# Performance work log

Measured on AMD Instinct MI355X. Metric: run time of the kernel, lower is better.

Reference implementation:

```python
import jax, jax.numpy as jnp
import numpy as np

N_NODES = 20000
N_EDGES = 320000
HEADS = 16
NEG_SLOPE = 0.2


def _gat_conv(x, src, dst, W, a_src, a_dst, b, heads, out_ch):
    # x: [N, F_in]; src/dst: [E'] (self-loops already appended)
    N = x.shape[0]
    h = (x @ W).reshape(N, heads, out_ch)                  # [N, H, C]
    alpha_s = jnp.sum(h * a_src, axis=-1)                  # [N, H]
    alpha_d = jnp.sum(h * a_dst, axis=-1)                  # [N, H]
    e = jax.nn.leaky_relu(alpha_s[src] + alpha_d[dst], NEG_SLOPE)  # [E', H]
    # segment softmax over edges grouped by destination node
    m = jax.ops.segment_max(e, dst, num_segments=N)        # [N, H]
    ex = jnp.exp(e - m[dst])
    denom = jax.ops.segment_sum(ex, dst, num_segments=N)
    alpha = ex / (denom[dst] + 1e-16)                      # [E', H]
    msg = h[src] * alpha[:, :, None]                       # [E', H, C]
    out = jax.ops.segment_sum(msg, dst, num_segments=N)    # [N, H, C]
    return out.reshape(N, heads * out_ch) + b


def _forward(x, edge_index, params):
    N = x.shape[0]
    loops = jnp.arange(N, dtype=edge_index.dtype)
    src = jnp.concatenate([edge_index[0], loops])
    dst = jnp.concatenate([edge_index[1], loops])
    for i, (W, a_s, a_d, b, out_ch) in enumerate(params):
        x = _gat_conv(x, src, dst, W, a_s, a_d, b, HEADS, out_ch)
        if i < len(params) - 1:
            x = jax.nn.relu(x)
    return jnp.sum(x, axis=0, keepdims=True)               # [1, 768]


def setup_inputs() -> dict:
    key = jax.random.key(0)
    ks = jax.random.split(key, 32)
    hid, heads, out_c = 64, HEADS, 3
    dims = [(3, hid), (hid * heads, hid), (hid * heads, hid), (hid * heads, hid), (hid * heads, hid), (hid * heads, out_c * heads)]
    inp = {}
    inp["x"] = jax.random.normal(ks[0], (N_NODES, 3), dtype=jnp.float32)
    inp["edge_index"] = jax.random.randint(ks[1], (2, N_EDGES), 0, N_NODES, dtype=jnp.int64)
    k = 2
    for li, (fin, c) in enumerate(dims, start=1):
        inp[f"W{li}"] = jax.random.normal(ks[k], (fin, heads * c), dtype=jnp.float32) * 0.1; k += 1
        inp[f"a{li}s"] = jax.random.normal(ks[k], (heads, c), dtype=jnp.float32) * 0.1; k += 1
        inp[f"a{li}d"] = jax.random.normal(ks[k], (heads, c), dtype=jnp.float32) * 0.1; k += 1
        inp[f"b{li}"] = jnp.zeros((heads * c,), dtype=jnp.float32)
    return inp


def reference(x, edge_index, W1, a1s, a1d, b1, W2, a2s, a2d, b2, W3, a3s, a3d, b3, W4, a4s, a4d, b4, W5, a5s, a5d, b5, W6, a6s, a6d, b6):
    params = [
        (W1, a1s, a1d, b1, 64), (W2, a2s, a2d, b2, 64), (W3, a3s, a3d, b3, 64),
        (W4, a4s, a4d, b4, 64), (W5, a5s, a5d, b5, 64), (W6, a6s, a6d, b6, 48),
    ]
    return _forward(x, edge_index, params)
```

## Files before the change

### kernel.cpp

```cpp
#include <hip/hip_runtime.h>
#include <cstddef>
#include <cstdint>

#define N_NODES 20000
#define N_EDGES 320000
#define E_TOT   (N_EDGES + N_NODES)
#define HEADS   16

typedef __bf16 bf16;
typedef __attribute__((ext_vector_type(8))) __bf16 bf16x8;
typedef __attribute__((ext_vector_type(4))) __bf16 bf16x4;
typedef __attribute__((ext_vector_type(4))) float  f32x4;

__device__ __forceinline__ void gll16(const void* g, void* l) {
    __builtin_amdgcn_global_load_lds(
        (const __attribute__((address_space(1))) unsigned int*)g,
        (__attribute__((address_space(3))) unsigned int*)l, 16, 0, 0);
}

__global__ __launch_bounds__(256)
void k_lin1(const float* __restrict__ x, const float* __restrict__ W,
            const float* __restrict__ aS, const float* __restrict__ aD,
            bf16* __restrict__ hg, float* __restrict__ as_,
            float* __restrict__ ad_) {
    int n = blockIdx.x;
    int t = threadIdx.x;
    int f0 = t * 4, hd = t >> 4;
    float x0 = x[n*3+0], x1 = x[n*3+1], x2 = x[n*3+2];
    float v[4];
    bf16x4 hv;
#pragma unroll
    for (int c = 0; c < 4; ++c) {
        int f = f0 + c;
        v[c] = x0*W[f] + x1*W[1024+f] + x2*W[2048+f];
        hv[c] = (bf16)v[c];
    }
    *reinterpret_cast<bf16x4*>(&hg[(size_t)n * 1024 + f0]) = hv;
    float ps = 0.f, pd = 0.f;
    int cb = (t & 15) * 4;
#pragma unroll
    for (int c = 0; c < 4; ++c) {
        ps = fmaf(v[c], aS[hd*64 + cb + c], ps);
        pd = fmaf(v[c], aD[hd*64 + cb + c], pd);
    }
#pragma unroll
    for (int off = 1; off < 16; off <<= 1) {
        ps += __shfl_xor(ps, off);
        pd += __shfl_xor(pd, off);
    }
    if ((t & 15) == 0) {
        as_[n*16 + hd] = ps;
        ad_[n*16 + hd] = pd;
    }
}

__global__ __launch_bounds__(256)
void k_convW(const float* __restrict__ W, bf16* __restrict__ Th,
             bf16* __restrict__ Tl, int M) {
    __shared__ float t[32][33];
    int m0 = blockIdx.x * 32, k0 = blockIdx.y * 32;
    int j = threadIdx.x & 31, i0 = threadIdx.x >> 5;
#pragma unroll
    for (int s = 0; s < 4; ++s) {
        int i = i0 + s * 8;
        t[i][j] = W[(size_t)(k0 + i) * M + m0 + j];
    }
    __syncthreads();
#pragma unroll
    for (int s = 0; s < 4; ++s) {
        int i = i0 + s * 8;
        float v = t[j][i];
        bf16 hi = (bf16)v;
        Th[(size_t)(m0 + i) * 1024 + k0 + j] = hi;
        if (Tl) Tl[(size_t)(m0 + i) * 1024 + k0 + j] = (bf16)(v - (float)hi);
    }
}

template<bool FUSE, bool TWOB>
__global__ __launch_bounds__(256, 2)
void k_gemm3(const bf16* __restrict__ Ah,
             const bf16* __restrict__ Bh, const bf16* __restrict__ Bl,
             float* __restrict__ Cf, bf16* __restrict__ Ch,
             const float* __restrict__ aS, const float* __restrict__ aD,
             float* __restrict__ as_, float* __restrict__ ad_,
             int N, int M) {
    __shared__ __align__(16) bf16 sAh[128 * 32];
    __shared__ __align__(16) bf16 sBh[128 * 32];
    __shared__ __align__(16) bf16 sBl[TWOB ? 128 * 32 : 8];

    const int tid  = threadIdx.x;
    const int wid  = tid >> 6, lane = tid & 63;
    const int wr   = wid >> 1, wc = wid & 1;
    const int col0 = blockIdx.x * 128, row0 = blockIdx.y * 128;

    f32x4 acc[4][4] = {};

    const int rl = lane >> 2;
    const int gg = lane & 3;
    const int rb0 = wid * 32;
    const int lrow = lane & 15, g4 = lane >> 4;

    for (int k0 = 0; k0 < 1024; k0 += 32) {
#pragma unroll
        for (int half = 0; half < 2; ++half) {
            int rt = rb0 + half * 16 + rl;
            int kc = (gg ^ ((rt >> 1) & 3)) * 8;
            size_t lbase = (size_t)(rb0 + half * 16) * 32;
            int ar = row0 + rt; if (ar >= N) ar = N - 1;
            gll16(Ah + (size_t)ar * 1024 + k0 + kc, sAh + lbase);
            int br = col0 + rt;
            gll16(Bh + (size_t)br * 1024 + k0 + kc, sBh + lbase);
            if (TWOB) gll16(Bl + (size_t)br * 1024 + k0 + kc, sBl + lbase);
        }
        __syncthreads();

        bf16x8 ah[4], bh[4], bl[4];
#pragma unroll
        for (int m = 0; m < 4; ++m) {
            int r = wr * 64 + m * 16 + lrow;
            int off = r * 32 + ((g4 ^ ((r >> 1) & 3)) * 8);
            ah[m] = *(const bf16x8*)&sAh[off];
        }
#pragma unroll
        for (int n = 0; n < 4; ++n) {
            int r = wc * 64 + n * 16 + lrow;
            int off = r * 32 + ((g4 ^ ((r >> 1) & 3)) * 8);
            bh[n] = *(const bf16x8*)&sBh[off];
            if (TWOB) bl[n] = *(const bf16x8*)&sBl[off];
        }
#pragma unroll
        for (int m = 0; m < 4; ++m)
#pragma unroll
            for (int n = 0; n < 4; ++n) {
                acc[m][n] = __builtin_amdgcn_mfma_f32_16x16x32_bf16(ah[m], bh[n], acc[m][n], 0, 0, 0);
                if (TWOB)
                    acc[m][n] = __builtin_amdgcn_mfma_f32_16x16x32_bf16(ah[m], bl[n], acc[m][n], 0, 0, 0);
            }
        __syncthreads();
    }

#pragma unroll
    for (int m = 0; m < 4; ++m) {
#pragma unroll
        for (int n = 0; n < 4; ++n) {
            int col = col0 + wc * 64 + n * 16 + lrow;
#pragma unroll
            for (int q = 0; q < 4; ++q) {
                int row = row0 + wr * 64 + m * 16 + g4 * 4 + q;
                if (row < N) {
                    float v = acc[m][n][q];
                    if (!FUSE) Cf[(size_t)row * M + col] = v;
                    Ch[(size_t)row * M + col] = (bf16)v;
                }
            }
        }
    }

    if (FUSE) {
        const int hd = blockIdx.x * 2 + wc;
        float asv[4], adv[4];
#pragma unroll
        for (int n = 0; n < 4; ++n) {
            asv[n] = aS[hd * 64 + n * 16 + lrow];
            adv[n] = aD[hd * 64 + n * 16 + lrow];
        }
        float ps[4][4], pd[4][4];
#pragma unroll
        for (int m = 0; m < 4; ++m)
#pragma unroll
            for (int q = 0; q < 4; ++q) {
                float s = 0.f, d = 0.f;
#pragma unroll
                for (int n = 0; n < 4; ++n) {
                    s = fmaf(acc[m][n][q], asv[n], s);
                    d = fmaf(acc[m][n][q], adv[n], d);
                }
                ps[m][q] = s; pd[m][q] = d;
            }
#pragma unroll
        for (int off = 1; off < 16; off <<= 1) {
#pragma unroll
            for (int m = 0; m < 4; ++m)
#pragma unroll
                for (int q = 0; q < 4; ++q) {
                    ps[m][q] += __shfl_xor(ps[m][q], off);
                    pd[m][q] += __shfl_xor(pd[m][q], off);
                }
        }
        if (lrow == 0) {
#pragma unroll
            for (int m = 0; m < 4; ++m)
#pragma unroll
                for (int q = 0; q < 4; ++q) {
                    int row = row0 + wr * 64 + m * 16 + g4 * 4 + q;
                    if (row < N) {
                        as_[row * 16 + hd] = ps[m][q];
                        ad_[row * 16 + hd] = pd[m][q];
                    }
                }
        }
    }
}

__global__ __launch_bounds__(256)
void k_alpha(const float* __restrict__ h, const float* __restrict__ a_s,
             const float* __restrict__ a_d, float* __restrict__ as_out,
             float* __restrict__ ad_out, int C, int M) {
    int pair = blockIdx.x * 4 + (threadIdx.x >> 6);
    int lane = threadIdx.x & 63;
    if (pair >= N_NODES * HEADS) return;
    int n = pair >> 4, hd = pair & 15;
    float vs = 0.f, vd = 0.f;
    if (lane < C) {
        float hv = h[(size_t)n * M + hd * C + lane];
        vs = hv * a_s[hd * C + lane];
        vd = hv * a_d[hd * C + lane];
    }
#pragma unroll
    for (int off = 32; off > 0; off >>= 1) {
        vs += __shfl_down(vs, off);
        vd += __shfl_down(vd, off);
    }
    if (lane == 0) { as_out[pair] = vs; ad_out[pair] = vd; }
}

__global__ void k_zero_i(int* __restrict__ p, int n) {
    int t = blockIdx.x * 256 + threadIdx.x;
    if (t < n) p[t] = 0;
}
__global__ void k_hist(const int* __restrict__ ei, int* __restrict__ deg) {
    int e = blockIdx.x * 256 + threadIdx.x;
    if (e >= E_TOT) return;
    int d = (e < N_EDGES) ? ei[N_EDGES + e] : e - N_EDGES;
    atomicAdd(&deg[d], 1);
}
__global__ __launch_bounds__(256)
void k_scan(const int* __restrict__ deg, int* __restrict__ rowstart,
            int* __restrict__ cursor) {
    __shared__ int sh[256];
    int carry = 0;
    for (int base = 0; base < N_NODES; base += 256) {
        int i = base + threadIdx.x;
        int v = (i < N_NODES) ? deg[i] : 0;
        sh[threadIdx.x] = v;
        __syncthreads();
        for (int off = 1; off < 256; off <<= 1) {
            int t = (threadIdx.x >= off) ? sh[threadIdx.x - off] : 0;
            __syncthreads();
            sh[threadIdx.x] += t;
            __syncthreads();
        }
        if (i < N_NODES) {
            int excl = carry + sh[threadIdx.x] - v;
            rowstart[i] = excl;
            cursor[i] = excl;
        }
        carry += sh[255];
        __syncthreads();
    }
    if (threadIdx.x == 0) rowstart[N_NODES] = carry;
}
__global__ void k_scatter(const int* __restrict__ ei, int* __restrict__ cursor,
                          int* __restrict__ csr_src) {
    int e = blockIdx.x * 256 + threadIdx.x;
    if (e >= E_TOT) return;
    int s, d;
    if (e < N_EDGES) { s = ei[e]; d = ei[N_EDGES + e]; }
    else             { s = d = e - N_EDGES; }
    int slot = atomicAdd(&cursor[d], 1);
    csr_src[slot] = s;
}

__global__ __launch_bounds__(256)
void k_agg1024(const bf16* __restrict__ hg, const int* __restrict__ rowstart,
               const int* __restrict__ csr_src, const float* __restrict__ as_,
               const float* __restrict__ ad_, const float* __restrict__ bias,
               bf16* __restrict__ oh) {
    int slice = blockIdx.x;
    int n = blockIdx.y * 16 + (threadIdx.x >> 4);
    int sub = threadIdx.x & 15;
    int f0 = slice * 128 + sub * 8;
    int hd = f0 >> 6;
    int s0 = rowstart[n], s1 = rowstart[n + 1];
    float adv = ad_[n * 16 + hd];
    float m = -1e30f, den = 0.f;
    float acc[8] = {};
    for (int j = s0; j < s1; ++j) {
        int s = csr_src[j];
        float v = as_[s * 16 + hd] + adv;
        v = v > 0.f ? v : 0.2f * v;
        bf16x8 hv = *reinterpret_cast<const bf16x8*>(&hg[(size_t)s * 1024 + f0]);
        float nm = fmaxf(m, v);
        float rm = __expf(m - nm);
        float re = __expf(v - nm);
        den = den * rm + re;
#pragma unroll
        for (int c = 0; c < 8; ++c)
            acc[c] = fmaf(acc[c], rm, re * (float)hv[c]);
        m = nm;
    }
    float inv = 1.f / (den + 1e-16f);
    bf16x8 vh;
#pragma unroll
    for (int c = 0; c < 8; ++c) {
        float r = fmaxf(fmaf(acc[c], inv, bias[f0 + c]), 0.f);
        vh[c] = (bf16)r;
    }
    *reinterpret_cast<bf16x8*>(&oh[(size_t)n * 1024 + f0]) = vh;
}

__global__ __launch_bounds__(256)
void k_agg768(const bf16* __restrict__ hg, const int* __restrict__ rowstart,
              const int* __restrict__ csr_src, const float* __restrict__ as_,
              const float* __restrict__ ad_, const float* __restrict__ bias,
              float* __restrict__ out) {
    int n = blockIdx.x * 2 + (threadIdx.x >> 7);
    int tloc = threadIdx.x & 127;
    if (tloc >= 96) return;
    int f0 = tloc * 8;
    int hd = f0 / 48;
    int s0 = rowstart[n], s1 = rowstart[n + 1];
    float adv = ad_[n * 16 + hd];
    float m = -1e30f, den = 0.f;
    float acc[8] = {};
    for (int j = s0; j < s1; ++j) {
        int s = csr_src[j];
        float v = as_[s * 16 + hd] + adv;
        v = v > 0.f ? v : 0.2f * v;
        bf16x8 hv = *reinterpret_cast<const bf16x8*>(&hg[(size_t)s * 768 + f0]);
        float nm = fmaxf(m, v);
        float rm = __expf(m - nm);
        float re = __expf(v - nm);
        den = den * rm + re;
#pragma unroll
        for (int c = 0; c < 8; ++c)
            acc[c] = fmaf(acc[c], rm, re * (float)hv[c]);
        m = nm;
    }
    float inv = 1.f / (den + 1e-16f);
#pragma unroll
    for (int c = 0; c < 8; ++c)
        out[(size_t)n * 768 + f0 + c] = fmaf(acc[c], inv, bias[f0 + c]);
}

__global__ __launch_bounds__(256)
void k_colsum(const float* __restrict__ x, float* __restrict__ out) {
    int f = blockIdx.x * 256 + threadIdx.x;
    int chunk = blockIdx.y;
    int n0 = chunk * 625, n1 = n0 + 625;
    float s = 0.f;
    for (int n = n0; n < n1; ++n) s += x[(size_t)n * 768 + f];
    atomicAdd(&out[f], s);
}

extern "C" void kernel_launch(void* const* d_in, const int* in_sizes, int n_in,
                              void* d_out, int out_size, void* d_ws, size_t ws_size,
                              hipStream_t stream) {
    const float* x0 = (const float*)d_in[0];
    const int*   ei = (const int*)d_in[1];

    char* w = (char*)d_ws;
    float* xB  = (float*)w;
    float* xOut = (float*)w;
    w += (size_t)N_NODES * 1024 * sizeof(float);
    bf16*  hgat = (bf16*)w; w += (size_t)N_NODES * 1024 * sizeof(bf16);
    bf16*  x_hi = (bf16*)w; w += (size_t)N_NODES * 1024 * sizeof(bf16);
    float* as_  = (float*)w; w += (size_t)N_NODES * HEADS * sizeof(float);
    float* ad_  = (float*)w; w += (size_t)N_NODES * HEADS * sizeof(float);
    bf16* Wt_hi = (bf16*)w; w += (size_t)1024 * 1024 * sizeof(bf16);
    bf16* Wt_lo = (bf16*)w; w += (size_t)1024 * 1024 * sizeof(bf16);
    int* deg      = (int*)w; w += N_NODES * sizeof(int);
    int* rowstart = (int*)w; w += (N_NODES + 1) * sizeof(int);
    int* cursor   = (int*)w; w += N_NODES * sizeof(int);
    int* csr_src  = (int*)w; w += E_TOT * sizeof(int);

    k_zero_i<<<(N_NODES + 255) / 256, 256, 0, stream>>>(deg, N_NODES);
    k_hist<<<(E_TOT + 255) / 256, 256, 0, stream>>>(ei, deg);
    k_scan<<<1, 256, 0, stream>>>(deg, rowstart, cursor);
    k_scatter<<<(E_TOT + 255) / 256, 256, 0, stream>>>(ei, cursor, csr_src);

    for (int l = 0; l < 6; ++l) {
        const float* W  = (const float*)d_in[2 + 4 * l + 0];
        const float* aS = (const float*)d_in[2 + 4 * l + 1];
        const float* aD = (const float*)d_in[2 + 4 * l + 2];
        const float* bv = (const float*)d_in[2 + 4 * l + 3];
        int M = (l == 5) ? 768 : 1024;

        if (l == 0) {
            k_lin1<<<N_NODES, 256, 0, stream>>>(x0, W, aS, aD, hgat, as_, ad_);
        } else {
            dim3 tg(M / 32, 32);
            dim3 grid(M / 128, (N_NODES + 127) / 128);
            if (l < 5) {
                k_convW<<<tg, 256, 0, stream>>>(W, Wt_hi, nullptr, M);
                k_gemm3<true, false><<<grid, 256, 0, stream>>>(
                    x_hi, Wt_hi, nullptr, nullptr, hgat, aS, aD, as_, ad_,
                    N_NODES, M);
            } else {
                k_convW<<<tg, 256, 0, stream>>>(W, Wt_hi, Wt_lo, M);
                k_gemm3<false, true><<<grid, 256, 0, stream>>>(
                    x_hi, Wt_hi, Wt_lo, xB, hgat, nullptr, nullptr,
                    nullptr, nullptr, N_NODES, M);
                k_alpha<<<(N_NODES * HEADS + 3) / 4, 256, 0, stream>>>(
                    xB, aS, aD, as_, ad_, 48, 768);
            }
        }
        if (l < 5) {
            dim3 agrid(8, N_NODES / 16);
            k_agg1024<<<agrid, 256, 0, stream>>>(
                hgat, rowstart, csr_src, as_, ad_, bv, x_hi);
        } else {
            k_agg768<<<N_NODES / 2, 256, 0, stream>>>(
                hgat, rowstart, csr_src, as_, ad_, bv, xOut);
        }
    }

    hipMemsetAsync(d_out, 0, (size_t)out_size * sizeof(float), stream);
    dim3 cgrid(3, 32);
    k_colsum<<<cgrid, 256, 0, stream>>>(xOut, (float*)d_out);
}
```

Measured before the change: 1.218 ms.

## Sort nodes by degree for aggregation and software-pipeline neighbor loads

```diff
diff --git a/kernel.cpp b/kernel.cpp
--- a/kernel.cpp
+++ b/kernel.cpp
@@ -271,33 +271,78 @@
     csr_src[slot] = s;
 }
 
+__global__ void k_dhist(const int* __restrict__ deg, int* __restrict__ bins) {
+    int n = blockIdx.x * 256 + threadIdx.x;
+    if (n >= N_NODES) return;
+    int d = deg[n]; if (d > 255) d = 255;
+    atomicAdd(&bins[d], 1);
+}
+__global__ __launch_bounds__(256)
+void k_dscan(const int* __restrict__ bins, int* __restrict__ cur) {
+    __shared__ int sh[256];
+    int v = bins[threadIdx.x];
+    sh[threadIdx.x] = v;
+    __syncthreads();
+    for (int off = 1; off < 256; off <<= 1) {
+        int t = (threadIdx.x >= off) ? sh[threadIdx.x - off] : 0;
+        __syncthreads();
+        sh[threadIdx.x] += t;
+        __syncthreads();
+    }
+    cur[threadIdx.x] = sh[threadIdx.x] - v;
+}
+__global__ void k_dscatter(const int* __restrict__ deg, int* __restrict__ cur,
+                           int* __restrict__ perm) {
+    int n = blockIdx.x * 256 + threadIdx.x;
+    if (n >= N_NODES) return;
+    int d = deg[n]; if (d > 255) d = 255;
+    int slot = atomicAdd(&cur[d], 1);
+    perm[slot] = n;
+}
+
 __global__ __launch_bounds__(256)
 void k_agg1024(const bf16* __restrict__ hg, const int* __restrict__ rowstart,
-               const int* __restrict__ csr_src, const float* __restrict__ as_,
-               const float* __restrict__ ad_, const float* __restrict__ bias,
-               bf16* __restrict__ oh) {
-    int slice = blockIdx.x;
-    int n = blockIdx.y * 16 + (threadIdx.x >> 4);
+               const int* __restrict__ csr_src, const int* __restrict__ perm,
+               const float* __restrict__ as_, const float* __restrict__ ad_,
+               const float* __restrict__ bias, bf16* __restrict__ oh) {
+    int n = perm[blockIdx.y * 16 + (threadIdx.x >> 4)];
     int sub = threadIdx.x & 15;
-    int f0 = slice * 128 + sub * 8;
+    int f0 = blockIdx.x * 128 + sub * 8;
     int hd = f0 >> 6;
     int s0 = rowstart[n], s1 = rowstart[n + 1];
     float adv = ad_[n * 16 + hd];
+
+    int s_cur = csr_src[s0];
+    float as_cur = as_[s_cur * 16 + hd];
+    bf16x8 hv_cur = *reinterpret_cast<const bf16x8*>(&hg[(size_t)s_cur * 1024 + f0]);
+    int jn = (s0 + 1 < s1) ? s0 + 1 : s1 - 1;
+    int s_nxt = csr_src[jn];
+
     float m = -1e30f, den = 0.f;
     float acc[8] = {};
     for (int j = s0; j < s1; ++j) {
-        int s = csr_src[j];
-        float v = as_[s * 16 + hd] + adv;
+        int j2 = (j + 2 < s1) ? j + 2 : s1 - 1;
+        int s_n2 = csr_src[j2];
+        float as_nxt = as_[s_nxt * 16 + hd];
+        bf16x8 hv_nxt = *reinterpret_cast<const bf16x8*>(&hg[(size_t)s_nxt * 1024 + f0]);
+
+        float v = as_cur + adv;
         v = v > 0.f ? v : 0.2f * v;
-        bf16x8 hv = *reinterpret_cast<const bf16x8*>(&hg[(size_t)s * 1024 + f0]);
-        float nm = fmaxf(m, v);
-        float rm = __expf(m - nm);
-        float re = __expf(v - nm);
-        den = den * rm + re;
-#pragma unroll
-        for (int c = 0; c < 8; ++c)
-            acc[c] = fmaf(acc[c], rm, re * (float)hv[c]);
-        m = nm;
+        if (v <= m) {
+            float re = __expf(v - m);
+            den += re;
+#pragma unroll
+            for (int c = 0; c < 8; ++c)
+                acc[c] = fmaf(re, (float)hv_cur[c], acc[c]);
+        } else {
+            float rm = __expf(m - v);
+            den = fmaf(den, rm, 1.f);
+#pragma unroll
+            for (int c = 0; c < 8; ++c)
+                acc[c] = fmaf(acc[c], rm, (float)hv_cur[c]);
+            m = v;
+        }
+        s_cur = s_nxt; as_cur = as_nxt; hv_cur = hv_nxt; s_nxt = s_n2;
     }
     float inv = 1.f / (den + 1e-16f);
     bf16x8 vh;
@@ -311,31 +356,48 @@
 
 __global__ __launch_bounds__(256)
 void k_agg768(const bf16* __restrict__ hg, const int* __restrict__ rowstart,
-              const int* __restrict__ csr_src, const float* __restrict__ as_,
-              const float* __restrict__ ad_, const float* __restrict__ bias,
-              float* __restrict__ out) {
-    int n = blockIdx.x * 2 + (threadIdx.x >> 7);
+              const int* __restrict__ csr_src, const int* __restrict__ perm,
+              const float* __restrict__ as_, const float* __restrict__ ad_,
+              const float* __restrict__ bias, float* __restrict__ out) {
+    int n = perm[blockIdx.x * 2 + (threadIdx.x >> 7)];
     int tloc = threadIdx.x & 127;
     if (tloc >= 96) return;
     int f0 = tloc * 8;
     int hd = f0 / 48;
     int s0 = rowstart[n], s1 = rowstart[n + 1];
     float adv = ad_[n * 16 + hd];
+
+    int s_cur = csr_src[s0];
+    float as_cur = as_[s_cur * 16 + hd];
+    bf16x8 hv_cur = *reinterpret_cast<const bf16x8*>(&hg[(size_t)s_cur * 768 + f0]);
+    int jn = (s0 + 1 < s1) ? s0 + 1 : s1 - 1;
+    int s_nxt = csr_src[jn];
+
     float m = -1e30f, den = 0.f;
     float acc[8] = {};
     for (int j = s0; j < s1; ++j) {
-        int s = csr_src[j];
-        float v = as_[s * 16 + hd] + adv;
+        int j2 = (j + 2 < s1) ? j + 2 : s1 - 1;
+        int s_n2 = csr_src[j2];
+        float as_nxt = as_[s_nxt * 16 + hd];
+        bf16x8 hv_nxt = *reinterpret_cast<const bf16x8*>(&hg[(size_t)s_nxt * 768 + f0]);
+
+        float v = as_cur + adv;
         v = v > 0.f ? v : 0.2f * v;
-        bf16x8 hv = *reinterpret_cast<const bf16x8*>(&hg[(size_t)s * 768 + f0]);
-        float nm = fmaxf(m, v);
-        float rm = __expf(m - nm);
-        float re = __expf(v - nm);
-        den = den * rm + re;
-#pragma unroll
-        for (int c = 0; c < 8; ++c)
-            acc[c] = fmaf(acc[c], rm, re * (float)hv[c]);
-        m = nm;
+        if (v <= m) {
+            float re = __expf(v - m);
+            den += re;
+#pragma unroll
+            for (int c = 0; c < 8; ++c)
+                acc[c] = fmaf(re, (float)hv_cur[c], acc[c]);
+        } else {
+            float rm = __expf(m - v);
+            den = fmaf(den, rm, 1.f);
+#pragma unroll
+            for (int c = 0; c < 8; ++c)
+                acc[c] = fmaf(acc[c], rm, (float)hv_cur[c]);
+            m = v;
+        }
+        s_cur = s_nxt; as_cur = as_nxt; hv_cur = hv_nxt; s_nxt = s_n2;
     }
     float inv = 1.f / (den + 1e-16f);
 #pragma unroll
@@ -373,11 +435,18 @@
     int* rowstart = (int*)w; w += (N_NODES + 1) * sizeof(int);
     int* cursor   = (int*)w; w += N_NODES * sizeof(int);
     int* csr_src  = (int*)w; w += E_TOT * sizeof(int);
+    int* dbins    = (int*)w; w += 256 * sizeof(int);
+    int* dcur     = (int*)w; w += 256 * sizeof(int);
+    int* perm     = (int*)w; w += N_NODES * sizeof(int);
 
     k_zero_i<<<(N_NODES + 255) / 256, 256, 0, stream>>>(deg, N_NODES);
     k_hist<<<(E_TOT + 255) / 256, 256, 0, stream>>>(ei, deg);
     k_scan<<<1, 256, 0, stream>>>(deg, rowstart, cursor);
     k_scatter<<<(E_TOT + 255) / 256, 256, 0, stream>>>(ei, cursor, csr_src);
+    k_zero_i<<<1, 256, 0, stream>>>(dbins, 256);
+    k_dhist<<<(N_NODES + 255) / 256, 256, 0, stream>>>(deg, dbins);
+    k_dscan<<<1, 256, 0, stream>>>(dbins, dcur);
+    k_dscatter<<<(N_NODES + 255) / 256, 256, 0, stream>>>(deg, dcur, perm);
 
     for (int l = 0; l < 6; ++l) {
         const float* W  = (const float*)d_in[2 + 4 * l + 0];
@@ -408,10 +477,10 @@
         if (l < 5) {
             dim3 agrid(8, N_NODES / 16);
             k_agg1024<<<agrid, 256, 0, stream>>>(
-                hgat, rowstart, csr_src, as_, ad_, bv, x_hi);
+                hgat, rowstart, csr_src, perm, as_, ad_, bv, x_hi);
         } else {
             k_agg768<<<N_NODES / 2, 256, 0, stream>>>(
-                hgat, rowstart, csr_src, as_, ad_, bv, xOut);
+                hgat, rowstart, csr_src, perm, as_, ad_, bv, xOut);
         }
     }
 
```

After: 1.247 ms. +2.4%, slower.

## Precompute per-edge softmax attention weights in a separate kernel before aggregation

Applied to the files above, without the earlier changes.

```diff
diff --git a/kernel.cpp b/kernel.cpp
--- a/kernel.cpp
+++ b/kernel.cpp
@@ -272,38 +272,55 @@
 }
 
 __global__ __launch_bounds__(256)
-void k_agg1024(const bf16* __restrict__ hg, const int* __restrict__ rowstart,
-               const int* __restrict__ csr_src, const float* __restrict__ as_,
-               const float* __restrict__ ad_, const float* __restrict__ bias,
-               bf16* __restrict__ oh) {
-    int slice = blockIdx.x;
-    int n = blockIdx.y * 16 + (threadIdx.x >> 4);
-    int sub = threadIdx.x & 15;
-    int f0 = slice * 128 + sub * 8;
-    int hd = f0 >> 6;
+void k_alpha_edge(const int* __restrict__ rowstart, const int* __restrict__ csr_src,
+                  const float* __restrict__ as_, const float* __restrict__ ad_,
+                  float* __restrict__ alpha) {
+    int t = blockIdx.x * 256 + threadIdx.x;
+    if (t >= N_NODES * HEADS) return;
+    int n = t >> 4, hd = t & 15;
     int s0 = rowstart[n], s1 = rowstart[n + 1];
-    float adv = ad_[n * 16 + hd];
+    float adv = ad_[t];
     float m = -1e30f, den = 0.f;
-    float acc[8] = {};
     for (int j = s0; j < s1; ++j) {
-        int s = csr_src[j];
-        float v = as_[s * 16 + hd] + adv;
+        float v = as_[csr_src[j] * 16 + hd] + adv;
         v = v > 0.f ? v : 0.2f * v;
-        bf16x8 hv = *reinterpret_cast<const bf16x8*>(&hg[(size_t)s * 1024 + f0]);
         float nm = fmaxf(m, v);
         float rm = __expf(m - nm);
         float re = __expf(v - nm);
         den = den * rm + re;
+        m = nm;
+    }
+    float inv = 1.f / (den + 1e-16f);
+    for (int j = s0; j < s1; ++j) {
+        float v = as_[csr_src[j] * 16 + hd] + adv;
+        v = v > 0.f ? v : 0.2f * v;
+        alpha[(size_t)j * 16 + hd] = __expf(v - m) * inv;
+    }
+}
+
+__global__ __launch_bounds__(256)
+void k_agg1024(const bf16* __restrict__ hg, const int* __restrict__ rowstart,
+               const int* __restrict__ csr_src, const float* __restrict__ alpha,
+               const float* __restrict__ bias, bf16* __restrict__ oh) {
+    int n = blockIdx.y * 16 + (threadIdx.x >> 4);
+    int sub = threadIdx.x & 15;
+    int f0 = blockIdx.x * 128 + sub * 8;
+    int hd = f0 >> 6;
+    int s0 = rowstart[n], s1 = rowstart[n + 1];
+    float acc[8] = {};
+#pragma unroll 2
+    for (int j = s0; j < s1; ++j) {
+        int s = csr_src[j];
+        float a = alpha[(size_t)j * 16 + hd];
+        bf16x8 hv = *reinterpret_cast<const bf16x8*>(&hg[(size_t)s * 1024 + f0]);
 #pragma unroll
         for (int c = 0; c < 8; ++c)
-            acc[c] = fmaf(acc[c], rm, re * (float)hv[c]);
-        m = nm;
-    }
-    float inv = 1.f / (den + 1e-16f);
+            acc[c] = fmaf(a, (float)hv[c], acc[c]);
+    }
     bf16x8 vh;
 #pragma unroll
     for (int c = 0; c < 8; ++c) {
-        float r = fmaxf(fmaf(acc[c], inv, bias[f0 + c]), 0.f);
+        float r = fmaxf(acc[c] + bias[f0 + c], 0.f);
         vh[c] = (bf16)r;
     }
     *reinterpret_cast<bf16x8*>(&oh[(size_t)n * 1024 + f0]) = vh;
@@ -311,36 +328,27 @@
 
 __global__ __launch_bounds__(256)
 void k_agg768(const bf16* __restrict__ hg, const int* __restrict__ rowstart,
-              const int* __restrict__ csr_src, const float* __restrict__ as_,
-              const float* __restrict__ ad_, const float* __restrict__ bias,
-              float* __restrict__ out) {
+              const int* __restrict__ csr_src, const float* __restrict__ alpha,
+              const float* __restrict__ bias, float* __restrict__ out) {
     int n = blockIdx.x * 2 + (threadIdx.x >> 7);
     int tloc = threadIdx.x & 127;
     if (tloc >= 96) return;
     int f0 = tloc * 8;
     int hd = f0 / 48;
     int s0 = rowstart[n], s1 = rowstart[n + 1];
-    float adv = ad_[n * 16 + hd];
-    float m = -1e30f, den = 0.f;
     float acc[8] = {};
+#pragma unroll 2
     for (int j = s0; j < s1; ++j) {
         int s = csr_src[j];
-        float v = as_[s * 16 + hd] + adv;
-        v = v > 0.f ? v : 0.2f * v;
+        float a = alpha[(size_t)j * 16 + hd];
         bf16x8 hv = *reinterpret_cast<const bf16x8*>(&hg[(size_t)s * 768 + f0]);
-        float nm = fmaxf(m, v);
-        float rm = __expf(m - nm);
-        float re = __expf(v - nm);
-        den = den * rm + re;
 #pragma unroll
         for (int c = 0; c < 8; ++c)
-            acc[c] = fmaf(acc[c], rm, re * (float)hv[c]);
-        m = nm;
-    }
-    float inv = 1.f / (den + 1e-16f);
+            acc[c] = fmaf(a, (float)hv[c], acc[c]);
+    }
 #pragma unroll
     for (int c = 0; c < 8; ++c)
-        out[(size_t)n * 768 + f0 + c] = fmaf(acc[c], inv, bias[f0 + c]);
+        out[(size_t)n * 768 + f0 + c] = acc[c] + bias[f0 + c];
 }
 
 __global__ __launch_bounds__(256)
@@ -367,6 +375,7 @@
     bf16*  x_hi = (bf16*)w; w += (size_t)N_NODES * 1024 * sizeof(bf16);
     float* as_  = (float*)w; w += (size_t)N_NODES * HEADS * sizeof(float);
     float* ad_  = (float*)w; w += (size_t)N_NODES * HEADS * sizeof(float);
+    float* alpha = (float*)w; w += (size_t)E_TOT * HEADS * sizeof(float);
     bf16* Wt_hi = (bf16*)w; w += (size_t)1024 * 1024 * sizeof(bf16);
     bf16* Wt_lo = (bf16*)w; w += (size_t)1024 * 1024 * sizeof(bf16);
     int* deg      = (int*)w; w += N_NODES * sizeof(int);
@@ -405,13 +414,15 @@
                     xB, aS, aD, as_, ad_, 48, 768);
             }
         }
+        k_alpha_edge<<<(N_NODES * HEADS + 255) / 256, 256, 0, stream>>>(
+            rowstart, csr_src, as_, ad_, alpha);
         if (l < 5) {
             dim3 agrid(8, N_NODES / 16);
             k_agg1024<<<agrid, 256, 0, stream>>>(
-                hgat, rowstart, csr_src, as_, ad_, bv, x_hi);
+                hgat, rowstart, csr_src, alpha, bv, x_hi);
         } else {
             k_agg768<<<N_NODES / 2, 256, 0, stream>>>(
-                hgat, rowstart, csr_src, as_, ad_, bv, xOut);
+                hgat, rowstart, csr_src, alpha, bv, xOut);
         }
     }
 
```

Result: slower. 1.297 ms (+6.5%).
